# Performance work log

Hardware: AMD Instinct MI355X
Metric: run time of the kernel (lower is better)

## Reference

```python
import jax, jax.numpy as jnp
import numpy as np

B, T, D, H = 4, 1024, 1024, 16
HD = D // H
DFF = 2048          # ExpertTier hidden width
K = 3               # ConvTier causal kernel size
NEG = -1e9


def layernorm(x, w, b, eps=1e-5):
    m = jnp.mean(x, axis=-1, keepdims=True)
    v = jnp.var(x, axis=-1, keepdims=True)
    return (x - m) * jax.lax.rsqrt(v + eps) * w + b


def rope_cos_sin(t, hd):
    inv = 1.0 / (10000.0 ** (jnp.arange(0, hd, 2, dtype=jnp.float32) / hd))
    freqs = jnp.outer(jnp.arange(t, dtype=jnp.float32), inv)  # (T, hd/2)
    return jnp.cos(freqs), jnp.sin(freqs)


def apply_rope(x, cos, sin):
    # x: (B, H, T, hd); cos/sin: (T, hd/2)
    x1, x2 = jnp.split(x, 2, axis=-1)
    return jnp.concatenate([x1 * cos - x2 * sin, x1 * sin + x2 * cos], axis=-1)


def causal_attn(q, k, v):
    # q,k,v: (..., T, d); full causal softmax attention
    t = q.shape[-2]
    scale = 1.0 / jnp.sqrt(jnp.asarray(q.shape[-1], q.dtype))
    scores = jnp.einsum('...qd,...kd->...qk', q, k) * scale
    mask = jnp.triu(jnp.ones((t, t), dtype=bool), k=1)
    scores = jnp.where(mask, NEG, scores)
    w = jax.nn.softmax(scores, axis=-1)
    return jnp.einsum('...qk,...kd->...qd', w, v)


def setup_inputs() -> dict:
    key = jax.random.key(0)
    ks = jax.random.split(key, 16)
    ws = 0.02
    g = lambda k, shape, s: jax.random.normal(k, shape, dtype=jnp.float32) * s
    return {
        'x': g(ks[0], (B, T, D), 1.0),
        'ln1_w': jnp.ones((D,), jnp.float32), 'ln1_b': jnp.zeros((D,), jnp.float32),
        'qkv_w': g(ks[1], (D, 3 * D), ws),
        'out_w': g(ks[2], (D, D), ws),
        'ln2_w': jnp.ones((D,), jnp.float32), 'ln2_b': jnp.zeros((D,), jnp.float32),
        'router_w': g(ks[3], (D, 4), ws),
        'conv_w': g(ks[4], (D, 1, K), 0.1),             # depthwise OIW, groups=D
        'expert_w1': g(ks[5], (D, DFF), ws),
        'expert_w2': g(ks[6], (DFF, D), ws),
        'at_wq': g(ks[7], (D, D), ws),
        'at_wk': g(ks[8], (D, D), ws),
        'at_wv': g(ks[9], (D, D), ws),
        'at_wo': g(ks[10], (D, D), ws),
        'tier_gate': jnp.full((D,), 0.1, jnp.float32),
        'sink_kv_scale': jnp.asarray(0.1, jnp.float32),
    }


def reference(x, ln1_w, ln1_b, qkv_w, out_w, ln2_w, ln2_b, router_w, conv_w,
              expert_w1, expert_w2, at_wq, at_wk, at_wv, at_wo,
              tier_gate, sink_kv_scale):
    b, t, d = x.shape
    # --- backbone causal self-attention with RoPE (pre-norm) ---
    h1 = layernorm(x, ln1_w, ln1_b)
    qkv = (h1 @ qkv_w).reshape(b, t, 3, H, HD)
    q = qkv[:, :, 0].transpose(0, 2, 1, 3)  # (B,H,T,hd)
    k = qkv[:, :, 1].transpose(0, 2, 1, 3)
    v = qkv[:, :, 2].transpose(0, 2, 1, 3)
    cos, sin = rope_cos_sin(t, HD)
    q = apply_rope(q, cos, sin)
    k = apply_rope(k, cos, sin)
    ao = causal_attn(q, k, v)                         # (B,H,T,hd)
    ao = ao.transpose(0, 2, 1, 3).reshape(b, t, d) @ out_w
    x = x + ao
    # --- router + tiers ---
    h = layernorm(x, ln2_w, ln2_b)
    routing_w = jax.nn.softmax(h @ router_w, axis=-1)  # (B,T,4): conv/expert/attn/sink
    # ConvTier: depthwise causal conv (k=3) + GELU
    hc = jnp.pad(h.transpose(0, 2, 1), ((0, 0), (0, 0), (K - 1, 0)))  # (B,D,T+K-1)
    conv = jax.lax.conv_general_dilated(hc, conv_w, (1,), 'VALID',
                                        feature_group_count=d,
                                        dimension_numbers=('NCH', 'OIH', 'NCH'))
    conv_out = jax.nn.gelu(conv.transpose(0, 2, 1))   # (B,T,D)
    # ExpertTier: 2-layer GELU MLP
    expert_out = jax.nn.gelu(h @ expert_w1) @ expert_w2
    # AttentionTier: single-head causal attention
    attn2 = causal_attn(h @ at_wq, h @ at_wk, h @ at_wv) @ at_wo
    # SinkTier outputs zeros -> contributes nothing to the weighted sum
    combined = (conv_out * routing_w[..., 0:1]
                + expert_out * routing_w[..., 1:2]
                + attn2 * routing_w[..., 2:3])
    x = x + combined * tier_gate
    # sink kv scaling
    kv_scale = 1.0 - routing_w[..., 3] * (1.0 - jnp.abs(sink_kv_scale))
    x = x * kv_scale[..., None]
    return (x, routing_w)
```

## Files before the change

### kernel.cpp

```cpp
#include <hip/hip_runtime.h>

#define Bz 4
#define Tz 1024
#define Dz 1024
#define Hz 16
#define NTz (Bz*Tz)

typedef short s8v __attribute__((ext_vector_type(8)));
typedef float f4v __attribute__((ext_vector_type(4)));

__device__ __forceinline__ float bf2f(unsigned short u){
  unsigned int x = ((unsigned int)u) << 16;
  return __builtin_bit_cast(float, x);
}
__device__ __forceinline__ unsigned short f2bf(float f){
  unsigned int x = __builtin_bit_cast(unsigned int, f);
  x += 0x7fffu + ((x >> 16) & 1u);
  return (unsigned short)(x >> 16);
}
__device__ __forceinline__ float gelu_f(float x){
  float z = 1.5957691216057308f * (x + 0.044715f * x * x * x);
  return x / (1.0f + __expf(-z));
}
__device__ __forceinline__ void gl16(const unsigned short* g, unsigned short* l){
  __builtin_amdgcn_global_load_lds(
      (const __attribute__((address_space(1))) unsigned int*)g,
      (__attribute__((address_space(3))) unsigned int*)l, 16, 0, 0);
}

#define VM(n) asm volatile("s_waitcnt vmcnt(" #n ")" ::: "memory")
#define BAR() asm volatile("s_barrier" ::: "memory")

struct WSeg { const float* in; unsigned short* out; int R, C, blk0, bx; };
struct WPack { WSeg s[8]; };
__global__ __launch_bounds__(256) void k_convtrans_all(WPack p)
{
  __shared__ float tile[32][33];
  int bid = blockIdx.x;
  const float* in = p.s[0].in; unsigned short* out = p.s[0].out;
  int R = p.s[0].R, C = p.s[0].C, blk0 = 0, bx = p.s[0].bx;
  #pragma unroll
  for (int i = 1; i < 8; ++i) {
    if (bid >= p.s[i].blk0) {
      in = p.s[i].in; out = p.s[i].out; R = p.s[i].R; C = p.s[i].C;
      blk0 = p.s[i].blk0; bx = p.s[i].bx;
    }
  }
  int rel = bid - blk0;
  int c0 = (rel % bx) * 32, r0 = (rel / bx) * 32;
  int tx = threadIdx.x & 31, ty = threadIdx.x >> 5;
  #pragma unroll
  for (int i = 0; i < 32; i += 8)
    tile[ty + i][tx] = in[(long)(r0 + ty + i) * C + c0 + tx];
  __syncthreads();
  #pragma unroll
  for (int i = 0; i < 32; i += 8)
    out[(long)(c0 + ty + i) * R + r0 + tx] = f2bf(tile[tx][ty + i]);
}

__global__ __launch_bounds__(256) void k_convtrans_b(const unsigned short* __restrict__ in,
    unsigned short* __restrict__ out, int ld, long sIn, long sOut)
{
  __shared__ unsigned short tile[32][34];
  in  += (long)blockIdx.z * sIn;
  out += (long)blockIdx.z * sOut;
  int c0 = blockIdx.x * 32, r0 = blockIdx.y * 32;
  int tx = threadIdx.x & 31, ty = threadIdx.x >> 5;
  #pragma unroll
  for (int i = 0; i < 32; i += 8)
    tile[ty + i][tx] = in[(long)(r0 + ty + i) * ld + c0 + tx];
  __syncthreads();
  #pragma unroll
  for (int i = 0; i < 32; i += 8)
    out[(long)(c0 + ty + i) * 1024 + r0 + tx] = tile[tx][ty + i];
}

__global__ __launch_bounds__(256) void k_layernorm(const float* __restrict__ x,
    const float* __restrict__ w, const float* __restrict__ b,
    unsigned short* __restrict__ out)
{
  int row = blockIdx.x, tid = threadIdx.x;
  const float4* xp = (const float4*)(x + (long)row * Dz);
  float4 v = xp[tid];
  float s  = v.x + v.y + v.z + v.w;
  float ss = v.x*v.x + v.y*v.y + v.z*v.z + v.w*v.w;
  int lane = tid & 63, wv = tid >> 6;
  #pragma unroll
  for (int off = 32; off; off >>= 1){ s += __shfl_xor(s, off); ss += __shfl_xor(ss, off); }
  __shared__ float red[8];
  if (lane == 0){ red[wv] = s; red[4 + wv] = ss; }
  __syncthreads();
  s  = red[0] + red[1] + red[2] + red[3];
  ss = red[4] + red[5] + red[6] + red[7];
  float mean = s * (1.0f / Dz);
  float var  = ss * (1.0f / Dz) - mean * mean;
  float rstd = rsqrtf(var + 1e-5f);
  float4 wg = ((const float4*)w)[tid];
  float4 bg = ((const float4*)b)[tid];
  ushort4 ov;
  ov.x = f2bf((v.x - mean) * rstd * wg.x + bg.x);
  ov.y = f2bf((v.y - mean) * rstd * wg.y + bg.y);
  ov.z = f2bf((v.z - mean) * rstd * wg.z + bg.z);
  ov.w = f2bf((v.w - mean) * rstd * wg.w + bg.w);
  *((ushort4*)(out + (long)row * Dz) + tid) = ov;
}

__global__ __launch_bounds__(256) void k_ln_router(const unsigned short* __restrict__ x2,
    const float* __restrict__ w, const float* __restrict__ b,
    const float* __restrict__ rw, unsigned short* __restrict__ out,
    float* __restrict__ rout)
{
  int row = blockIdx.x, tid = threadIdx.x;
  ushort4 xu = *((const ushort4*)(x2 + (long)row * Dz) + tid);
  float4 v = {bf2f(xu.x), bf2f(xu.y), bf2f(xu.z), bf2f(xu.w)};
  float s  = v.x + v.y + v.z + v.w;
  float ss = v.x*v.x + v.y*v.y + v.z*v.z + v.w*v.w;
  int lane = tid & 63, wv = tid >> 6;
  #pragma unroll
  for (int off = 32; off; off >>= 1){ s += __shfl_xor(s, off); ss += __shfl_xor(ss, off); }
  __shared__ float red[8];
  if (lane == 0){ red[wv] = s; red[4 + wv] = ss; }
  __syncthreads();
  s  = red[0] + red[1] + red[2] + red[3];
  ss = red[4] + red[5] + red[6] + red[7];
  float mean = s * (1.0f / Dz);
  float var  = ss * (1.0f / Dz) - mean * mean;
  float rstd = rsqrtf(var + 1e-5f);
  float4 wg = ((const float4*)w)[tid];
  float4 bg = ((const float4*)b)[tid];
  float h0 = (v.x - mean) * rstd * wg.x + bg.x;
  float h1 = (v.y - mean) * rstd * wg.y + bg.y;
  float h2 = (v.z - mean) * rstd * wg.z + bg.z;
  float h3 = (v.w - mean) * rstd * wg.w + bg.w;
  ushort4 ov;
  ov.x = f2bf(h0); ov.y = f2bf(h1); ov.z = f2bf(h2); ov.w = f2bf(h3);
  *((ushort4*)(out + (long)row * Dz) + tid) = ov;
  int d0 = tid * 4;
  float4 r0 = *(const float4*)(rw + (long)d0 * 4);
  float4 r1 = *(const float4*)(rw + (long)(d0 + 1) * 4);
  float4 r2 = *(const float4*)(rw + (long)(d0 + 2) * 4);
  float4 r3 = *(const float4*)(rw + (long)(d0 + 3) * 4);
  float a0 = h0*r0.x + h1*r1.x + h2*r2.x + h3*r3.x;
  float a1 = h0*r0.y + h1*r1.y + h2*r2.y + h3*r3.y;
  float a2 = h0*r0.z + h1*r1.z + h2*r2.z + h3*r3.z;
  float a3 = h0*r0.w + h1*r1.w + h2*r2.w + h3*r3.w;
  #pragma unroll
  for (int off = 32; off; off >>= 1) {
    a0 += __shfl_xor(a0, off); a1 += __shfl_xor(a1, off);
    a2 += __shfl_xor(a2, off); a3 += __shfl_xor(a3, off);
  }
  __shared__ float red2[4][4];
  if (lane == 0){ red2[wv][0] = a0; red2[wv][1] = a1; red2[wv][2] = a2; red2[wv][3] = a3; }
  __syncthreads();
  if (tid == 0) {
    float s0 = red2[0][0] + red2[1][0] + red2[2][0] + red2[3][0];
    float s1 = red2[0][1] + red2[1][1] + red2[2][1] + red2[3][1];
    float s2 = red2[0][2] + red2[1][2] + red2[2][2] + red2[3][2];
    float s3 = red2[0][3] + red2[1][3] + red2[2][3] + red2[3][3];
    float mx = fmaxf(fmaxf(s0, s1), fmaxf(s2, s3));
    float e0 = __expf(s0 - mx), e1 = __expf(s1 - mx);
    float e2 = __expf(s2 - mx), e3 = __expf(s3 - mx);
    float inv = 1.0f / (e0 + e1 + e2 + e3);
    float4 r = {e0 * inv, e1 * inv, e2 * inv, e3 * inv};
    *(float4*)(rout + (long)row * 4) = r;
  }
}

__global__ __launch_bounds__(256) void k_gemm3s(
    const unsigned short* __restrict__ A,
    const unsigned short* __restrict__ Bt,
    unsigned short* __restrict__ Cb)
{
  constexpr int BM = 64, BN = 128, BK = 64;
  __shared__ unsigned short As[3][BM * BK];
  __shared__ unsigned short Bs[3][BN * BK];
  int lin = blockIdx.y * gridDim.x + blockIdx.x;
  int cols = gridDim.x, rows = gridDim.y;
  int nwg = cols * rows;
  if ((nwg & 7) == 0) lin = (lin & 7) * (nwg >> 3) + (lin >> 3);
  int in_grp = 8 * cols;
  int gid = lin / in_grp;
  int fm = gid * 8;
  int gsz = min(rows - fm, 8);
  int rem = lin - gid * in_grp;
  int pm = fm + (rem % gsz);
  int pn = rem / gsz;
  int bm = pm * BM, bn = pn * BN;

  int tid = threadIdx.x, w = tid >> 6, lane = tid & 63;
  int fr = lane & 15, fg = lane >> 4;
  int sw = (fr & 7) * 8;
  int wc = w * 32;
  int lrow = lane >> 3;
  int lcol = ((lane & 7) ^ lrow) * 8;

  const unsigned short* AgJ[2];
  int AsOff[2];
  #pragma unroll
  for (int j = 0; j < 2; ++j) {
    AgJ[j] = A + (long)(bm + w * 16 + j * 8 + lrow) * 1024 + lcol;
    AsOff[j] = (w * 16 + j * 8) * BK;
  }
  const unsigned short* BgJ[4];
  int BsOff[4];
  #pragma unroll
  for (int j = 0; j < 4; ++j) {
    BgJ[j] = Bt + (long)(bn + w * 32 + j * 8 + lrow) * 1024 + lcol;
    BsOff[j] = (w * 32 + j * 8) * BK;
  }

  f4v acc[4][2];
  #pragma unroll
  for (int m = 0; m < 4; ++m)
    #pragma unroll
    for (int n = 0; n < 2; ++n)
      acc[m][n] = (f4v){0.f, 0.f, 0.f, 0.f};

  auto stage = [&](int buf, int kt){
    int k0 = kt * BK;
    #pragma unroll
    for (int j = 0; j < 2; ++j) gl16(AgJ[j] + k0, &As[buf][AsOff[j]]);
    #pragma unroll
    for (int j = 0; j < 4; ++j) gl16(BgJ[j] + k0, &Bs[buf][BsOff[j]]);
  };
  auto compute = [&](int buf){
    #pragma unroll
    for (int kk = 0; kk < 2; ++kk) {
      int kg = (kk * 32 + fg * 8) ^ sw;
      s8v af[4], bfv[2];
      #pragma unroll
      for (int m = 0; m < 4; ++m) af[m]  = *(const s8v*)&As[buf][(m * 16 + fr) * BK + kg];
      #pragma unroll
      for (int n = 0; n < 2; ++n) bfv[n] = *(const s8v*)&Bs[buf][(wc + n * 16 + fr) * BK + kg];
      #pragma unroll
      for (int m = 0; m < 4; ++m)
        #pragma unroll
        for (int n = 0; n < 2; ++n)
          acc[m][n] = __builtin_amdgcn_mfma_f32_16x16x32_bf16(af[m], bfv[n], acc[m][n], 0, 0, 0);
    }
  };

  stage(0, 0);
  stage(1, 1);
  VM(6); BAR();
  for (int k = 0; k < 14; ++k) {
    stage((k + 2) % 3, k + 2);
    VM(12); BAR();
    compute(k % 3);
    BAR();
  }
  VM(6); BAR(); compute(2); BAR();
  VM(0); BAR(); compute(0);

  int cr = bm + fg * 4, cc = bn + wc + fr;
  #pragma unroll
  for (int m = 0; m < 4; ++m)
    #pragma unroll
    for (int n = 0; n < 2; ++n)
      #pragma unroll
      for (int i = 0; i < 4; ++i) {
        long row = cr + m * 16 + i;
        long col = cc + n * 16;
        float v = acc[m][n][i];
        if (col < 2048) v = gelu_f(v);
        Cb[row * 5120 + col] = f2bf(v);
      }
}

template<int MODE, int BN, bool TRIMAP, bool TRIK, bool DBUF>
__global__ __launch_bounds__(256) void k_gemm(
    const unsigned short* __restrict__ A,
    const unsigned short* __restrict__ Bt,
    float* __restrict__ Cf, unsigned short* __restrict__ Cb,
    const float* __restrict__ addsrc,
    unsigned short* __restrict__ P1, unsigned short* __restrict__ P2,
    int N, int K, int lda, int ldb,
    long sA, long sB, long sC)
{
  constexpr int BM = 128;
  constexpr int MREP = (BN == 128) ? 4 : 2;
  constexpr int NB = DBUF ? 2 : 1;
  __shared__ unsigned short As[NB][BM * 64];
  __shared__ unsigned short Bs[NB][BN * 64];
  int bm, bn;
  if (TRIMAP) {
    int li = blockIdx.x;
    int nwg = gridDim.x;
    if ((nwg & 7) == 0) li = (li & 7) * (nwg >> 3) + (li >> 3);
    int r = (int)((sqrtf(4.f * li + 1.f) - 1.f) * 0.5f);
    if ((r + 1) * (r + 2) <= li) ++r;
    if (r * (r + 1) > li) --r;
    bm = r * 128; bn = (li - r * (r + 1)) * BN;
  } else {
    int lin = blockIdx.y * gridDim.x + blockIdx.x;
    int nwg = gridDim.x * gridDim.y;
    if ((nwg & 7) == 0) lin = (lin & 7) * (nwg >> 3) + (lin >> 3);
    int cols = gridDim.x, rows = gridDim.y;
    constexpr int GM = 8;
    int in_grp = GM * cols;
    int gid = lin / in_grp;
    int fm = gid * GM;
    int gsz = min(rows - fm, GM);
    int rem = lin - gid * in_grp;
    int pm = fm + (rem % gsz);
    int pn = rem / gsz;
    if (TRIK) pm = rows - 1 - pm;
    bm = pm * BM; bn = pn * BN;
  }
  A  += (long)blockIdx.z * sA;
  Bt += (long)blockIdx.z * sB;
  int tid = threadIdx.x, w = tid >> 6, lane = tid & 63;
  int wr, wc;
  if (BN == 128) { wr = (w >> 1) * 64; wc = (w & 1) * 64; }
  else           { wr = w * 32;        wc = 0; }
  f4v acc[MREP][4];
  #pragma unroll
  for (int m = 0; m < MREP; ++m)
    #pragma unroll
    for (int n = 0; n < 4; ++n)
      acc[m][n] = (f4v){0.f, 0.f, 0.f, 0.f};

  int Keff = K;
  if (TRIK) Keff = min(K, bm + BM);

  int lrow = lane >> 3;
  int lcol = (((lane & 7) ^ lrow) * 8);
  const unsigned short* AgJ[4];
  int AsOff[4];
  #pragma unroll
  for (int j = 0; j < 4; ++j) {
    AgJ[j] = A + (long)(bm + w * 32 + j * 8 + lrow) * lda + lcol;
    AsOff[j] = (w * 32 + j * 8) * 64;
  }
  constexpr int BCH = BN / 8 / 4;
  const unsigned short* BgJ[BCH];
  int BsOff[BCH];
  #pragma unroll
  for (int j = 0; j < BCH; ++j) {
    BgJ[j] = Bt + (long)(bn + w * (BCH * 8) + j * 8 + lrow) * ldb + lcol;
    BsOff[j] = (w * (BCH * 8) + j * 8) * 64;
  }

  int fr = lane & 15, fg = lane >> 4;
  int sw = (fr & 7) * 8;

  auto stage = [&](int buf, int k0){
    #pragma unroll
    for (int j = 0; j < 4; ++j) gl16(AgJ[j] + k0, &As[buf][AsOff[j]]);
    #pragma unroll
    for (int j = 0; j < BCH; ++j) gl16(BgJ[j] + k0, &Bs[buf][BsOff[j]]);
  };
  auto compute = [&](int buf){
    #pragma unroll
    for (int kk = 0; kk < 2; ++kk) {
      int kg = (kk * 32 + fg * 8) ^ sw;
      s8v af[MREP], bfv[4];
      #pragma unroll
      for (int m = 0; m < MREP; ++m) af[m]  = *(const s8v*)&As[buf][(wr + m * 16 + fr) * 64 + kg];
      #pragma unroll
      for (int n = 0; n < 4; ++n)    bfv[n] = *(const s8v*)&Bs[buf][(wc + n * 16 + fr) * 64 + kg];
      #pragma unroll
      for (int m = 0; m < MREP; ++m)
        #pragma unroll
        for (int n = 0; n < 4; ++n)
          acc[m][n] = __builtin_amdgcn_mfma_f32_16x16x32_bf16(af[m], bfv[n], acc[m][n], 0, 0, 0);
    }
  };

  if (DBUF) {
    int cur = 0;
    stage(0, 0);
    __syncthreads();
    for (int k0 = 0; k0 < Keff; k0 += 64) {
      if (k0 + 64 < Keff) stage(cur ^ 1, k0 + 64);
      compute(cur);
      __syncthreads();
      cur ^= 1;
    }
  } else {
    for (int k0 = 0; k0 < Keff; k0 += 64) {
      __syncthreads();
      stage(0, k0);
      __syncthreads();
      compute(0);
    }
  }

  int cr0 = bm + wr + fg * 4;
  int cc0 = bn + wc + fr;

  if (MODE == 4) {
    int sect = bn >> 10;
    if (sect == 2) {
      #pragma unroll
      for (int m = 0; m < MREP; ++m)
        #pragma unroll
        for (int n = 0; n < 4; ++n)
          #pragma unroll
          for (int i = 0; i < 4; ++i) {
            int row = cr0 + m * 16 + i;
            int vcol = (bn - 2048) + wc + n * 16 + fr;
            P2[(long)row * 1024 + vcol] = f2bf(acc[m][n][i]);
          }
    } else {
      unsigned short* dst = (sect == 0) ? Cb : P1;
      float scl = (sect == 0) ? 0.125f : 1.0f;
      int head = ((bn & 1023) + wc) >> 6;
      float inv0 = exp2f(-(float)fr * 0.4152410118609203f);
      float inv1 = exp2f(-(float)(fr + 16) * 0.4152410118609203f);
      #pragma unroll
      for (int m = 0; m < MREP; ++m)
        #pragma unroll
        for (int i = 0; i < 4; ++i) {
          int row = cr0 + m * 16 + i;
          int t = row & 1023, bq = row >> 10;
          float a0 = (float)t * inv0, a1 = (float)t * inv1;
          float cs0 = __cosf(a0), sn0 = __sinf(a0);
          float cs1 = __cosf(a1), sn1 = __sinf(a1);
          float v0 = acc[m][0][i], v1 = acc[m][1][i];
          float v2 = acc[m][2][i], v3 = acc[m][3][i];
          long base = ((long)(bq * 16 + head)) * 65536 + (long)t * 64 + fr;
          dst[base]      = f2bf((v0 * cs0 - v2 * sn0) * scl);
          dst[base + 32] = f2bf((v0 * sn0 + v2 * cs0) * scl);
          dst[base + 16] = f2bf((v1 * cs1 - v3 * sn1) * scl);
          dst[base + 48] = f2bf((v1 * sn1 + v3 * cs1) * scl);
        }
    }
    return;
  }

  #pragma unroll
  for (int m = 0; m < MREP; ++m)
    #pragma unroll
    for (int n = 0; n < 4; ++n)
      #pragma unroll
      for (int i = 0; i < 4; ++i) {
        long row = cr0 + m * 16 + i, col = cc0 + n * 16;
        long idx = (long)blockIdx.z * sC + row * (long)N + col;
        float v = acc[m][n][i];
        if (MODE == 1 || MODE == 7) v += addsrc[idx];
        if (MODE == 6) v *= 0.03125f;
        if (MODE <= 1) Cf[idx] = v; else Cb[idx] = f2bf(v);
      }
}

__global__ __launch_bounds__(256) void k_attn_mfma(
    const unsigned short* __restrict__ Qb, const unsigned short* __restrict__ Kb,
    const unsigned short* __restrict__ Vt, unsigned short* __restrict__ ao)
{
  __shared__ unsigned short Ks[64][72];
  __shared__ unsigned short Vs[64][72];
  __shared__ unsigned short Ps[4][16][72];
  int qb = 15 - (blockIdx.x >> 6);
  int bh = blockIdx.x & 63;
  int b = bh >> 4, h = bh & 15;
  int t0 = qb * 64;
  int tid = threadIdx.x, w = tid >> 6, lane = tid & 63;
  int fr = lane & 15, fg = lane >> 4;

  const unsigned short* qp = Qb + (long)bh * Tz * 64 + (long)(t0 + w * 16 + fr) * 64 + fg * 8;
  s8v qf[2] = { *(const s8v*)qp, *(const s8v*)(qp + 32) };

  f4v o_acc[4];
  #pragma unroll
  for (int n = 0; n < 4; ++n) o_acc[n] = (f4v){0.f, 0.f, 0.f, 0.f};
  float m_[4] = {-1e30f, -1e30f, -1e30f, -1e30f};
  float l_[4] = {0.f, 0.f, 0.f, 0.f};

  int sr = tid >> 3, sc = (tid & 7) * 8;
  const unsigned short* Kg = Kb + (long)bh * Tz * 64 + (long)sr * 64 + sc;
  const unsigned short* Vg = Vt + (long)bh * 64 * Tz + (long)sr * Tz + sc;

  uint4 pk0, pk1, pv0, pv1;
  auto loadregs = [&](int k0){
    pk0 = *(const uint4*)(Kg + (long)k0 * 64);
    pk1 = *(const uint4*)(Kg + (long)(k0 + 32) * 64);
    pv0 = *(const uint4*)(Vg + k0);
    pv1 = *(const uint4*)(Vg + (long)32 * Tz + k0);
  };
  auto storelds = [&](){
    *(uint4*)&Ks[sr][sc]      = pk0;
    *(uint4*)&Ks[sr + 32][sc] = pk1;
    *(uint4*)&Vs[sr][sc]      = pv0;
    *(uint4*)&Vs[sr + 32][sc] = pv1;
  };

  loadregs(0);
  storelds();
  __syncthreads();

  for (int kt = 0; kt <= qb; ++kt) {
    int k0 = kt * 64;
    if (kt < qb) loadregs(k0 + 64);

    f4v sacc[4];
    #pragma unroll
    for (int n = 0; n < 4; ++n) sacc[n] = (f4v){0.f, 0.f, 0.f, 0.f};
    #pragma unroll
    for (int kk = 0; kk < 2; ++kk) {
      int kg = kk * 32 + fg * 8;
      #pragma unroll
      for (int n = 0; n < 4; ++n) {
        s8v bf = *(const s8v*)&Ks[n * 16 + fr][kg];
        sacc[n] = __builtin_amdgcn_mfma_f32_16x16x32_bf16(qf[kk], bf, sacc[n], 0, 0, 0);
      }
    }

    bool full = (kt < qb);
    float p[4][4], alpha[4];
    #pragma unroll
    for (int i = 0; i < 4; ++i) {
      int trow = t0 + w * 16 + fg * 4 + i;
      float mx = -1e30f;
      #pragma unroll
      for (int n = 0; n < 4; ++n) {
        float sval = sacc[n][i];
        if (!full) {
          int key = k0 + n * 16 + fr;
          sval = (key <= trow) ? sval : -1e30f;
        }
        p[n][i] = sval;
        mx = fmaxf(mx, sval);
      }
      mx = fmaxf(mx, __shfl_xor(mx, 1));
      mx = fmaxf(mx, __shfl_xor(mx, 2));
      mx = fmaxf(mx, __shfl_xor(mx, 4));
      mx = fmaxf(mx, __shfl_xor(mx, 8));
      float mnew = fmaxf(m_[i], mx);
      alpha[i] = __expf(m_[i] - mnew);
      m_[i] = mnew;
      float ps = 0.f;
      #pragma unroll
      for (int n = 0; n < 4; ++n) {
        float pv = __expf(p[n][i] - mnew);
        p[n][i] = pv;
        ps += pv;
      }
      ps += __shfl_xor(ps, 1); ps += __shfl_xor(ps, 2);
      ps += __shfl_xor(ps, 4); ps += __shfl_xor(ps, 8);
      l_[i] = l_[i] * alpha[i] + ps;
    }
    #pragma unroll
    for (int n = 0; n < 4; ++n)
      #pragma unroll
      for (int i = 0; i < 4; ++i)
        o_acc[n][i] *= alpha[i];
    #pragma unroll
    for (int n = 0; n < 4; ++n)
      #pragma unroll
      for (int i = 0; i < 4; ++i)
        Ps[w][fg * 4 + i][n * 16 + fr] = f2bf(p[n][i]);

    #pragma unroll
    for (int kk = 0; kk < 2; ++kk) {
      int kg = kk * 32 + fg * 8;
      s8v pa = *(const s8v*)&Ps[w][fr][kg];
      #pragma unroll
      for (int n = 0; n < 4; ++n) {
        s8v vb = *(const s8v*)&Vs[n * 16 + fr][kg];
        o_acc[n] = __builtin_amdgcn_mfma_f32_16x16x32_bf16(pa, vb, o_acc[n], 0, 0, 0);
      }
    }

    if (kt < qb) {
      __syncthreads();
      storelds();
      __syncthreads();
    }
  }

  float inv[4];
  #pragma unroll
  for (int i = 0; i < 4; ++i) inv[i] = 1.0f / l_[i];
  #pragma unroll
  for (int n = 0; n < 4; ++n)
    #pragma unroll
    for (int i = 0; i < 4; ++i) {
      int t = t0 + w * 16 + fg * 4 + i;
      ao[((long)(b * Tz + t)) * Dz + h * 64 + n * 16 + fr] = f2bf(o_acc[n][i] * inv[i]);
    }
}

__global__ __launch_bounds__(256) void k_softmax_causal(const unsigned short* __restrict__ S,
    unsigned short* __restrict__ P)
{
  long row = blockIdx.x;
  int t = (int)(row & (Tz - 1));
  int tid = threadIdx.x;
  const unsigned short* sp = S + row * Tz;
  ushort4 v = ((const ushort4*)sp)[tid];
  float vv[4];
  vv[0] = (tid*4 + 0 <= t) ? bf2f(v.x) : -1e30f;
  vv[1] = (tid*4 + 1 <= t) ? bf2f(v.y) : -1e30f;
  vv[2] = (tid*4 + 2 <= t) ? bf2f(v.z) : -1e30f;
  vv[3] = (tid*4 + 3 <= t) ? bf2f(v.w) : -1e30f;
  float mx = fmaxf(fmaxf(vv[0], vv[1]), fmaxf(vv[2], vv[3]));
  int lane = tid & 63, wv = tid >> 6;
  #pragma unroll
  for (int off = 32; off; off >>= 1) mx = fmaxf(mx, __shfl_xor(mx, off));
  __shared__ float red[8];
  if (lane == 0) red[wv] = mx;
  __syncthreads();
  mx = fmaxf(fmaxf(red[0], red[1]), fmaxf(red[2], red[3]));
  float p[4];
  float s = 0.f;
  #pragma unroll
  for (int i = 0; i < 4; ++i){ p[i] = __expf(vv[i] - mx); s += p[i]; }
  #pragma unroll
  for (int off = 32; off; off >>= 1) s += __shfl_xor(s, off);
  if (lane == 0) red[4 + wv] = s;
  __syncthreads();
  s = red[4] + red[5] + red[6] + red[7];
  float inv = 1.0f / s;
  ushort4 ov;
  ov.x = f2bf(p[0] * inv); ov.y = f2bf(p[1] * inv);
  ov.z = f2bf(p[2] * inv); ov.w = f2bf(p[3] * inv);
  *((ushort4*)(P + row * Tz) + tid) = ov;
}

__global__ __launch_bounds__(256) void k_combine(
    const unsigned short* __restrict__ x2, const unsigned short* __restrict__ hbf,
    const unsigned short* __restrict__ eoa, const unsigned short* __restrict__ eob,
    const unsigned short* __restrict__ ap,
    const float* __restrict__ rout, const float* __restrict__ convw,
    const float* __restrict__ tg, const float* __restrict__ sinkp,
    float* __restrict__ outx)
{
  int row = blockIdx.x, tid = threadIdx.x;
  int t = row & (Tz - 1), b = row >> 10;
  int d0 = tid * 4;
  ushort4 xu = *(const ushort4*)(x2 + (long)row * Dz + d0);
  ushort4 ea = *(const ushort4*)(eoa + (long)row * Dz + d0);
  ushort4 eb = *(const ushort4*)(eob + (long)row * Dz + d0);
  ushort4 a4 = *(const ushort4*)(ap + (long)row * Dz + d0);
  float4 t4 = *(const float4*)(tg + d0);
  float4 r4 = *(const float4*)(rout + (long)row * 4);
  float sks = fabsf(sinkp[0]);
  float kv = 1.0f - r4.w * (1.0f - sks);
  const float4* cwp = (const float4*)(convw + (long)d0 * 3);
  float4 c0 = cwp[0], c1 = cwp[1], c2 = cwp[2];
  float cwf[12] = {c0.x, c0.y, c0.z, c0.w, c1.x, c1.y, c1.z, c1.w, c2.x, c2.y, c2.z, c2.w};
  float hv[3][4];
  #pragma unroll
  for (int tap = 0; tap < 3; ++tap) {
    int tt = t - 2 + tap;
    if (tt >= 0) {
      ushort4 hu = *((const ushort4*)(hbf + ((long)(b * Tz + tt)) * Dz + d0));
      hv[tap][0] = bf2f(hu.x); hv[tap][1] = bf2f(hu.y);
      hv[tap][2] = bf2f(hu.z); hv[tap][3] = bf2f(hu.w);
    } else {
      hv[tap][0] = 0.f; hv[tap][1] = 0.f; hv[tap][2] = 0.f; hv[tap][3] = 0.f;
    }
  }
  float ov[4];
  float xi[4] = {bf2f(xu.x), bf2f(xu.y), bf2f(xu.z), bf2f(xu.w)};
  float ei[4] = {bf2f(ea.x) + bf2f(eb.x), bf2f(ea.y) + bf2f(eb.y),
                 bf2f(ea.z) + bf2f(eb.z), bf2f(ea.w) + bf2f(eb.w)};
  float ai[4] = {bf2f(a4.x), bf2f(a4.y), bf2f(a4.z), bf2f(a4.w)};
  float ti[4] = {t4.x, t4.y, t4.z, t4.w};
  #pragma unroll
  for (int i = 0; i < 4; ++i) {
    float conv = hv[0][i] * cwf[i*3 + 0] + hv[1][i] * cwf[i*3 + 1] + hv[2][i] * cwf[i*3 + 2];
    float comb = gelu_f(conv) * r4.x + ei[i] * r4.y + ai[i] * r4.z;
    ov[i] = (xi[i] + comb * ti[i]) * kv;
  }
  float4 res = {ov[0], ov[1], ov[2], ov[3]};
  *(float4*)(outx + (long)row * Dz + d0) = res;
}

extern "C" void kernel_launch(void* const* d_in, const int* in_sizes, int n_in,
                              void* d_out, int out_size, void* d_ws, size_t ws_size,
                              hipStream_t stream) {
  (void)in_sizes; (void)n_in; (void)out_size; (void)ws_size;
  const float* x       = (const float*)d_in[0];
  const float* ln1_w   = (const float*)d_in[1];
  const float* ln1_b   = (const float*)d_in[2];
  const float* qkv_w   = (const float*)d_in[3];
  const float* out_w   = (const float*)d_in[4];
  const float* ln2_w   = (const float*)d_in[5];
  const float* ln2_b   = (const float*)d_in[6];
  const float* router_w= (const float*)d_in[7];
  const float* conv_w  = (const float*)d_in[8];
  const float* ew1     = (const float*)d_in[9];
  const float* ew2     = (const float*)d_in[10];
  const float* at_wq   = (const float*)d_in[11];
  const float* at_wk   = (const float*)d_in[12];
  const float* at_wv   = (const float*)d_in[13];
  const float* at_wo   = (const float*)d_in[14];
  const float* tg      = (const float*)d_in[15];
  const float* sinkp   = (const float*)d_in[16];
  float* outx = (float*)d_out;
  float* rout = outx + (size_t)NTz * Dz;

  char* ws = (char*)d_ws;
  size_t off = 0;
  auto alloc = [&](size_t bytes) -> char* {
    char* p = ws + off;
    off += (bytes + 255) & ~(size_t)255;
    return p;
  };
  const long TD = (long)Tz * Dz, TT = (long)Tz * Tz;

  unsigned short* w_qkvt  = (unsigned short*)alloc((size_t)3072*1024*2);
  unsigned short* w_outt  = (unsigned short*)alloc((size_t)1024*1024*2);
  unsigned short* w_tiert = (unsigned short*)alloc((size_t)5120*1024*2);
  unsigned short* w_ew2t  = (unsigned short*)alloc((size_t)1024*2048*2);
  unsigned short* w_wot   = (unsigned short*)alloc((size_t)1024*1024*2);
  unsigned short* h1bf    = (unsigned short*)alloc((size_t)NTz*Dz*2);
  unsigned short* tierb   = (unsigned short*)alloc((size_t)NTz*5120*2);
  unsigned short* aobf    = (unsigned short*)alloc((size_t)NTz*Dz*2);
  unsigned short* x2b     = (unsigned short*)alloc((size_t)NTz*Dz*2);
  unsigned short* hbf     = (unsigned short*)alloc((size_t)NTz*Dz*2);
  unsigned short* Pbf     = (unsigned short*)alloc((size_t)Bz*Tz*Tz*2);
  unsigned short* v2tbf   = (unsigned short*)alloc((size_t)NTz*Dz*2);
  unsigned short* a2obf   = (unsigned short*)alloc((size_t)NTz*Dz*2);
  unsigned short* eofb    = (unsigned short*)alloc((size_t)NTz*Dz*2);
  unsigned short* a2pb    = (unsigned short*)alloc((size_t)NTz*Dz*2);
  unsigned short* Sbf     = (unsigned short*)alloc((size_t)Bz*Tz*Tz*2);

  unsigned short* Qb = x2b;
  unsigned short* Kb = Pbf;
  unsigned short* Vb = tierb;
  unsigned short* Vt = a2pb;
  unsigned short* eofb2 = h1bf;
  long eoDelta = (long)(eofb2 - eofb);

  dim3 blk(256);

  WPack wp;
  wp.s[0] = {qkv_w, w_qkvt,                         1024, 3072, 0,     96};
  wp.s[1] = {out_w, w_outt,                         1024, 1024, 3072,  32};
  wp.s[2] = {ew1,   w_tiert,                        1024, 2048, 4096,  64};
  wp.s[3] = {at_wq, w_tiert + 2048*1024,            1024, 1024, 6144,  32};
  wp.s[4] = {at_wk, w_tiert + 3072*1024,            1024, 1024, 7168,  32};
  wp.s[5] = {at_wv, w_tiert + (size_t)4096*1024,    1024, 1024, 8192,  32};
  wp.s[6] = {ew2,   w_ew2t,                         2048, 1024, 9216,  32};
  wp.s[7] = {at_wo, w_wot,                          1024, 1024, 11264, 32};
  k_convtrans_all<<<dim3(12288), blk, 0, stream>>>(wp);

  k_layernorm<<<NTz, blk, 0, stream>>>(x, ln1_w, ln1_b, h1bf);
  k_gemm<4,128,false,false,true><<<dim3(24, 32), blk, 0, stream>>>(h1bf, w_qkvt,
      nullptr, Qb, nullptr, Kb, Vb, 3072, 1024, 1024, 1024, 0, 0, 0);
  k_convtrans_b<<<dim3(32, 32, 4), blk, 0, stream>>>(Vb, Vt, 1024, TD, TD);
  k_attn_mfma<<<dim3(1024), blk, 0, stream>>>(Qb, Kb, Vt, aobf);
  k_gemm<7,64,false,false,true><<<dim3(16, 32), blk, 0, stream>>>(aobf, w_outt, nullptr,
      x2b, x, nullptr, nullptr, 1024, 1024, 1024, 1024, 0, 0, 0);
  k_ln_router<<<NTz, blk, 0, stream>>>(x2b, ln2_w, ln2_b, router_w, hbf, rout);
  k_gemm3s<<<dim3(40, 64), blk, 0, stream>>>(hbf, w_tiert, tierb);
  k_gemm<3,64,false,false,true><<<dim3(16, 32, 2), blk, 0, stream>>>(tierb, w_ew2t,
      nullptr, eofb, nullptr, nullptr, nullptr, 1024, 1024, 5120, 2048,
      1024, 1024, eoDelta);
  k_convtrans_b<<<dim3(32, 32, 4), blk, 0, stream>>>(tierb + 4096, v2tbf, 5120,
      (long)Tz*5120, TD);
  k_gemm<6,64,true,false,true><<<dim3(72, 1, 4), blk, 0, stream>>>(tierb + 2048,
      tierb + 3072, nullptr, Sbf, nullptr, nullptr, nullptr,
      1024, 1024, 5120, 5120, (long)Tz*5120, (long)Tz*5120, TT);
  k_softmax_causal<<<NTz, blk, 0, stream>>>(Sbf, Pbf);
  k_gemm<3,64,false,true,true><<<dim3(16, 8, 4), blk, 0, stream>>>(Pbf, v2tbf, nullptr,
      a2obf, nullptr, nullptr, nullptr, 1024, 1024, 1024, 1024, TT, TD, TD);
  k_gemm<3,64,false,false,true><<<dim3(16, 32), blk, 0, stream>>>(a2obf, w_wot, nullptr,
      a2pb, nullptr, nullptr, nullptr, 1024, 1024, 1024, 1024, 0, 0, 0);
  k_combine<<<NTz, blk, 0, stream>>>(x2b, hbf, eofb, eofb2, a2pb, rout, conv_w,
      tg, sinkp, outx);
}
```

Measured before the change: 302.5 us.

## Use 128x128 tiles with 512 threads for the fused tier GEMM

Replaces the 64x128, 256-thread, three-stage tier projection GEMM with a 128x128 tile computed by 8 waves. Each wave now owns a 32x64 sub-tile. Staging is a two-buffer ping-pong synchronised with __syncthreads instead of explicit vmcnt waits. The larger tile raises data reuse per LDS load and halves the number of workgroups. In exchange it gives up the deeper three-stage prefetch, and every iteration now drains all outstanding loads at the barrier.

```diff
diff --git a/kernel.cpp b/kernel.cpp
--- a/kernel.cpp
+++ b/kernel.cpp
@@ -27,9 +27,6 @@
       (const __attribute__((address_space(1))) unsigned int*)g,
       (__attribute__((address_space(3))) unsigned int*)l, 16, 0, 0);
 }
-
-#define VM(n) asm volatile("s_waitcnt vmcnt(" #n ")" ::: "memory")
-#define BAR() asm volatile("s_barrier" ::: "memory")
 
 struct WSeg { const float* in; unsigned short* out; int R, C, blk0, bx; };
 struct WPack { WSeg s[8]; };
@@ -166,14 +163,14 @@
   }
 }
 
-__global__ __launch_bounds__(256) void k_gemm3s(
+__global__ __launch_bounds__(512) void k_gemm512(
     const unsigned short* __restrict__ A,
     const unsigned short* __restrict__ Bt,
     unsigned short* __restrict__ Cb)
 {
-  constexpr int BM = 64, BN = 128, BK = 64;
-  __shared__ unsigned short As[3][BM * BK];
-  __shared__ unsigned short Bs[3][BN * BK];
+  constexpr int BK = 64;
+  __shared__ unsigned short As[2][128 * BK];
+  __shared__ unsigned short Bs[2][128 * BK];
   int lin = blockIdx.y * gridDim.x + blockIdx.x;
   int cols = gridDim.x, rows = gridDim.y;
   int nwg = cols * rows;
@@ -185,78 +182,70 @@
   int rem = lin - gid * in_grp;
   int pm = fm + (rem % gsz);
   int pn = rem / gsz;
-  int bm = pm * BM, bn = pn * BN;
+  int bm = pm * 128, bn = pn * 128;
 
   int tid = threadIdx.x, w = tid >> 6, lane = tid & 63;
   int fr = lane & 15, fg = lane >> 4;
   int sw = (fr & 7) * 8;
-  int wc = w * 32;
+  int wr = (w >> 1) * 32, wc = (w & 1) * 64;
   int lrow = lane >> 3;
   int lcol = ((lane & 7) ^ lrow) * 8;
 
   const unsigned short* AgJ[2];
-  int AsOff[2];
+  const unsigned short* BgJ[2];
+  int OffJ[2];
   #pragma unroll
   for (int j = 0; j < 2; ++j) {
-    AgJ[j] = A + (long)(bm + w * 16 + j * 8 + lrow) * 1024 + lcol;
-    AsOff[j] = (w * 16 + j * 8) * BK;
-  }
-  const unsigned short* BgJ[4];
-  int BsOff[4];
-  #pragma unroll
-  for (int j = 0; j < 4; ++j) {
-    BgJ[j] = Bt + (long)(bn + w * 32 + j * 8 + lrow) * 1024 + lcol;
-    BsOff[j] = (w * 32 + j * 8) * BK;
-  }
-
-  f4v acc[4][2];
-  #pragma unroll
-  for (int m = 0; m < 4; ++m)
-    #pragma unroll
-    for (int n = 0; n < 2; ++n)
+    AgJ[j] = A  + (long)(bm + j * 64 + w * 8 + lrow) * 1024 + lcol;
+    BgJ[j] = Bt + (long)(bn + j * 64 + w * 8 + lrow) * 1024 + lcol;
+    OffJ[j] = (j * 64 + w * 8) * BK;
+  }
+
+  f4v acc[2][4];
+  #pragma unroll
+  for (int m = 0; m < 2; ++m)
+    #pragma unroll
+    for (int n = 0; n < 4; ++n)
       acc[m][n] = (f4v){0.f, 0.f, 0.f, 0.f};
 
-  auto stage = [&](int buf, int kt){
-    int k0 = kt * BK;
-    #pragma unroll
-    for (int j = 0; j < 2; ++j) gl16(AgJ[j] + k0, &As[buf][AsOff[j]]);
-    #pragma unroll
-    for (int j = 0; j < 4; ++j) gl16(BgJ[j] + k0, &Bs[buf][BsOff[j]]);
+  auto stage = [&](int buf, int k0){
+    #pragma unroll
+    for (int j = 0; j < 2; ++j) gl16(AgJ[j] + k0, &As[buf][OffJ[j]]);
+    #pragma unroll
+    for (int j = 0; j < 2; ++j) gl16(BgJ[j] + k0, &Bs[buf][OffJ[j]]);
   };
   auto compute = [&](int buf){
     #pragma unroll
     for (int kk = 0; kk < 2; ++kk) {
       int kg = (kk * 32 + fg * 8) ^ sw;
-      s8v af[4], bfv[2];
-      #pragma unroll
-      for (int m = 0; m < 4; ++m) af[m]  = *(const s8v*)&As[buf][(m * 16 + fr) * BK + kg];
-      #pragma unroll
-      for (int n = 0; n < 2; ++n) bfv[n] = *(const s8v*)&Bs[buf][(wc + n * 16 + fr) * BK + kg];
-      #pragma unroll
-      for (int m = 0; m < 4; ++m)
+      s8v af[2], bfv[4];
+      #pragma unroll
+      for (int m = 0; m < 2; ++m) af[m]  = *(const s8v*)&As[buf][(wr + m * 16 + fr) * BK + kg];
+      #pragma unroll
+      for (int n = 0; n < 4; ++n) bfv[n] = *(const s8v*)&Bs[buf][(wc + n * 16 + fr) * BK + kg];
+      #pragma unroll
+      for (int m = 0; m < 2; ++m)
         #pragma unroll
-        for (int n = 0; n < 2; ++n)
+        for (int n = 0; n < 4; ++n)
           acc[m][n] = __builtin_amdgcn_mfma_f32_16x16x32_bf16(af[m], bfv[n], acc[m][n], 0, 0, 0);
     }
   };
 
+  int cur = 0;
   stage(0, 0);
-  stage(1, 1);
-  VM(6); BAR();
-  for (int k = 0; k < 14; ++k) {
-    stage((k + 2) % 3, k + 2);
-    VM(12); BAR();
-    compute(k % 3);
-    BAR();
-  }
-  VM(6); BAR(); compute(2); BAR();
-  VM(0); BAR(); compute(0);
-
-  int cr = bm + fg * 4, cc = bn + wc + fr;
-  #pragma unroll
-  for (int m = 0; m < 4; ++m)
-    #pragma unroll
-    for (int n = 0; n < 2; ++n)
+  __syncthreads();
+  for (int k0 = 0; k0 < 1024; k0 += BK) {
+    if (k0 + BK < 1024) stage(cur ^ 1, k0 + BK);
+    compute(cur);
+    __syncthreads();
+    cur ^= 1;
+  }
+
+  int cr = bm + wr + fg * 4, cc = bn + wc + fr;
+  #pragma unroll
+  for (int m = 0; m < 2; ++m)
+    #pragma unroll
+    for (int n = 0; n < 4; ++n)
       #pragma unroll
       for (int i = 0; i < 4; ++i) {
         long row = cr + m * 16 + i;
@@ -746,7 +735,7 @@
   k_gemm<7,64,false,false,true><<<dim3(16, 32), blk, 0, stream>>>(aobf, w_outt, nullptr,
       x2b, x, nullptr, nullptr, 1024, 1024, 1024, 1024, 0, 0, 0);
   k_ln_router<<<NTz, blk, 0, stream>>>(x2b, ln2_w, ln2_b, router_w, hbf, rout);
-  k_gemm3s<<<dim3(40, 64), blk, 0, stream>>>(hbf, w_tiert, tierb);
+  k_gemm512<<<dim3(40, 32), dim3(512), 0, stream>>>(hbf, w_tiert, tierb);
   k_gemm<3,64,false,false,true><<<dim3(16, 32, 2), blk, 0, stream>>>(tierb, w_ew2t,
       nullptr, eofb, nullptr, nullptr, nullptr, 1024, 1024, 5120, 2048,
       1024, 1024, eoDelta);
```

Measured after the change: 285.8 us (median of 2 runs). 1.06x faster.
